# Optimization experiments

Measured on AMD Instinct MI355X. Metric: run time of the kernel, lower is better.

The kernel has to match this reference:

```python
import jax, jax.numpy as jnp
import numpy as np

DIM = 1024
H = 16
DH = DIM // H
SCALE = DH ** -0.5
EPS = 1e-5


def _linear_params(key, fan_in, fan_out):
    k1, k2 = jax.random.split(key)
    bound = 1.0 / np.sqrt(fan_in)
    w = jax.random.uniform(k1, (fan_out, fan_in), jnp.float32, -bound, bound)
    b = jax.random.uniform(k2, (fan_out,), jnp.float32, -bound, bound)
    return w, b


def setup_inputs() -> dict:
    key = jax.random.key(0)
    ks = jax.random.split(key, 16)
    M, K, S_txt, S_img = 32, 128, 1024, 768
    inp = {
        'entity_text': jax.random.normal(ks[0], (M, K, DIM), jnp.float32),
        'entity_image': jax.random.normal(ks[1], (M, K, DIM), jnp.float32),
        'img_feat': jax.random.normal(ks[2], (M, S_img, DIM), jnp.float32),
        'txt_feat': jax.random.normal(ks[3], (M, S_txt, DIM), jnp.float32),
    }
    img_mask = jax.random.randint(ks[4], (M, S_img), 0, 2, jnp.int32)
    txt_mask = jax.random.randint(ks[5], (M, S_txt), 0, 2, jnp.int32)
    # guarantee at least one valid kv token per row (avoids all -inf rows)
    inp['img_mask'] = img_mask.at[:, 0].set(1)
    inp['txt_mask'] = txt_mask.at[:, 0].set(1)
    names = ['wq_t', 'wk_t', 'wv_t', 'wo_t', 'wq_i', 'wk_i', 'wv_i', 'wo_i']
    for i, n in enumerate(names):
        w, b = _linear_params(ks[6 + i], DIM, DIM)
        inp[n] = w
        inp['b' + n[1:]] = b
    inp['g_t'] = jnp.ones((DIM,), jnp.float32)
    inp['beta_t'] = jnp.zeros((DIM,), jnp.float32)
    inp['g_i'] = jnp.ones((DIM,), jnp.float32)
    inp['beta_i'] = jnp.zeros((DIM,), jnp.float32)
    return inp


def _attend(wq, bq, wk, bk, wv, bv, wo, bo, queries, kv, kv_mask):
    M, K, D = queries.shape
    S = kv.shape[1]
    Q = (queries @ wq.T + bq).reshape(M, K, H, DH)
    Kt = (kv @ wk.T + bk).reshape(M, S, H, DH)
    V = (kv @ wv.T + bv).reshape(M, S, H, DH)
    attn = jnp.einsum('mkhd,mshd->mhks', Q, Kt) * SCALE  # [M,H,K,S]
    attn = jnp.where(kv_mask[:, None, None, :] > 0, attn, -jnp.inf)
    attn = jax.nn.softmax(attn, axis=-1)
    attn = jnp.nan_to_num(attn, nan=0.0)  # dropout=eval mode (identity)
    out = jnp.einsum('mhks,mshd->mkhd', attn, V).reshape(M, K, D)
    return out @ wo.T + bo


def _layernorm(x, g, b):
    mu = jnp.mean(x, axis=-1, keepdims=True)
    var = jnp.mean(jnp.square(x - mu), axis=-1, keepdims=True)
    return (x - mu) * jax.lax.rsqrt(var + EPS) * g + b


def reference(entity_text, entity_image, img_feat, txt_feat, img_mask, txt_mask,
              wq_t, bq_t, wk_t, bk_t, wv_t, bv_t, wo_t, bo_t,
              wq_i, bq_i, wk_i, bk_i, wv_i, bv_i, wo_i, bo_i,
              g_t, beta_t, g_i, beta_i):
    out_t = _attend(wq_t, bq_t, wk_t, bk_t, wv_t, bv_t, wo_t, bo_t,
                    entity_text, txt_feat, txt_mask)
    out_i = _attend(wq_i, bq_i, wk_i, bk_i, wv_i, bv_i, wo_i, bo_i,
                    entity_image, img_feat, img_mask)
    et = _layernorm(entity_text + out_t, g_t, beta_t)
    ei = _layernorm(entity_image + out_i, g_i, beta_i)
    return (et, ei)
```

## Files before the change

kernel.cpp:

```cpp
#include <hip/hip_runtime.h>
#include <stdint.h>

typedef unsigned short u16;
typedef __attribute__((ext_vector_type(8))) short short8;
typedef __attribute__((ext_vector_type(4))) float f32x4;

#define SWZ(r) (((r) & 7) << 4)
#define SCALE 0.125f

__device__ __forceinline__ u16 f2bf(float f) {
  unsigned int x = __float_as_uint(f);
  x += 0x7fffu + ((x >> 16) & 1u);
  return (u16)(x >> 16);
}

__device__ __forceinline__ unsigned int cvtpk_bf16(float lo, float hi) {
  unsigned int r;
  asm("v_cvt_pk_bf16_f32 %0, %1, %2" : "=v"(r) : "v"(lo), "v"(hi));
  return r;
}

__device__ __forceinline__ f32x4 mfma16(short8 a, short8 b, f32x4 c) {
  return __builtin_amdgcn_mfma_f32_16x16x32_bf16(a, b, c, 0, 0, 0);
}

__device__ __forceinline__ void gload_lds16(const u16* g, u16* l) {
  __builtin_amdgcn_global_load_lds(
      (const __attribute__((address_space(1))) unsigned int*)g,
      (__attribute__((address_space(3))) unsigned int*)l, 16, 0, 0);
}

__device__ __forceinline__ int xcd_swz(int bid, int nwg) {
  int cpx = nwg >> 3;
  return (bid & 7) * cpx + (bid >> 3);
}

__device__ __forceinline__ void cvt8(const float* src, u16* dst) {
  float4 a = *(const float4*)src;
  float4 b = *(const float4*)(src + 4);
  uint4 u;
  u.x = cvtpk_bf16(a.x, a.y);
  u.y = cvtpk_bf16(a.z, a.w);
  u.z = cvtpk_bf16(b.x, b.y);
  u.w = cvtpk_bf16(b.z, b.w);
  *(uint4*)dst = u;
}

__global__ __launch_bounds__(256) void cvt_all_kernel(
    const float* __restrict__ w0, const float* __restrict__ w1,
    const float* __restrict__ w2, const float* __restrict__ w3,
    const float* __restrict__ ent, const float* __restrict__ feat,
    u16* __restrict__ Wbf, u16* __restrict__ entbf, u16* __restrict__ featbf,
    int nE8, int nF8) {
  const int nW8 = 524288;
  int total = nW8 + nE8 + nF8;
  int i = blockIdx.x * 256 + threadIdx.x;
  int stride = gridDim.x * 256;
  for (; i < total; i += stride) {
    if (i < nW8) {
      int mi = i >> 17;
      const float* s = (mi == 0) ? w0 : (mi == 1) ? w1 : (mi == 2) ? w2 : w3;
      size_t off = (size_t)(i & 131071) * 8;
      cvt8(s + off, Wbf + (size_t)mi * 1048576 + off);
    } else if (i < nW8 + nE8) {
      size_t off = (size_t)(i - nW8) * 8;
      cvt8(ent + off, entbf + off);
    } else {
      size_t off = (size_t)(i - nW8 - nE8) * 8;
      cvt8(feat + off, featbf + off);
    }
  }
}

__global__ __launch_bounds__(256) void cvt_a_kernel(
    const float* __restrict__ src, u16* __restrict__ dst, int n8) {
  int i = blockIdx.x * 256 + threadIdx.x;
  int stride = gridDim.x * 256;
  for (; i < n8; i += stride) cvt8(src + (size_t)i * 8, dst + (size_t)i * 8);
}

__device__ __forceinline__ void gemm_core_bf16(
    const u16* __restrict__ A, const u16* __restrict__ B,
    const float* __restrict__ bias0, const float* __restrict__ bias1,
    u16* __restrict__ C, int ldc, int bx, int by, u16* As, u16* Bs) {
  const int tid = threadIdx.x;
  const int lane = tid & 63;
  const int w = tid >> 6;
  const int wr = w >> 1, wc = w & 1;
  const int l15 = lane & 15, lg = lane >> 4;
  const int brow = by * 128;
  const int bcol = bx * 128;

  f32x4 acc[4][4] = {};

  for (int k0 = 0; k0 < 1024; k0 += 64) {
#pragma unroll
    for (int p = 0; p < 4; ++p) {
      int flat = p * 256 + tid;
      int row = flat >> 3;
      int cb = (flat & 7) * 16;
      int scb = cb ^ SWZ(row);
      gload_lds16(B + (size_t)(bcol + row) * 1024 + k0 + (scb >> 1),
                  Bs + (size_t)flat * 8);
    }
#pragma unroll
    for (int p = 0; p < 4; ++p) {
      int flat = p * 256 + tid;
      int row = flat >> 3;
      int cb = (flat & 7) * 16;
      int scb = cb ^ SWZ(row);
      gload_lds16(A + (size_t)(brow + row) * 1024 + k0 + (scb >> 1),
                  As + (size_t)flat * 8);
    }
    __syncthreads();

    short8 af[4][2], bfr[4][2];
#pragma unroll
    for (int i = 0; i < 4; ++i) {
#pragma unroll
      for (int kk = 0; kk < 2; ++kk) {
        int ar = wr * 64 + i * 16 + l15;
        af[i][kk] = *(const short8*)((const char*)As + ar * 128 +
                                     ((kk * 64 + lg * 16) ^ SWZ(ar)));
        int br = wc * 64 + i * 16 + l15;
        bfr[i][kk] = *(const short8*)((const char*)Bs + br * 128 +
                                      ((kk * 64 + lg * 16) ^ SWZ(br)));
      }
    }
#pragma unroll
    for (int i = 0; i < 4; ++i)
#pragma unroll
      for (int j = 0; j < 4; ++j)
#pragma unroll
        for (int kk = 0; kk < 2; ++kk)
          acc[i][j] = mfma16(af[i][kk], bfr[j][kk], acc[i][j]);
    __syncthreads();
  }

#pragma unroll
  for (int j = 0; j < 4; ++j) {
    int col = bcol + wc * 64 + j * 16 + l15;
    const float* bp = (col < 1024) ? bias0 : bias1;
    float bv = bp[col & 1023];
#pragma unroll
    for (int i = 0; i < 4; ++i) {
      int row0 = brow + wr * 64 + i * 16 + lg * 4;
#pragma unroll
      for (int r = 0; r < 4; ++r)
        C[(size_t)(row0 + r) * ldc + col] = f2bf(acc[i][j][r] + bv);
    }
  }
}

__global__ __launch_bounds__(256, 2) void qkv_gemm_kernel(
    const u16* __restrict__ A0, const u16* __restrict__ B0,
    const float* __restrict__ bq, u16* __restrict__ C0, int gx0, int nwg0,
    const u16* __restrict__ A1, const u16* __restrict__ B1,
    const float* __restrict__ bk, const float* __restrict__ bv,
    u16* __restrict__ C1, int gx1, int nwg1) {
  __shared__ __attribute__((aligned(16))) u16 As[128 * 64];
  __shared__ __attribute__((aligned(16))) u16 Bs[128 * 64];
  int bid = blockIdx.x;
  if (bid < nwg0) {
    int lid = xcd_swz(bid, nwg0);
    gemm_core_bf16(A0, B0, bq, bq, C0, 1024, lid % gx0, lid / gx0, As, Bs);
  } else {
    int lid = xcd_swz(bid - nwg0, nwg1);
    gemm_core_bf16(A1, B1, bk, bv, C1, 2048, lid % gx1, lid / gx1, As, Bs);
  }
}

template <bool A_F32, bool OUT_F32>
__global__ __launch_bounds__(256, 2) void gemm_bias_kernel(
    const void* __restrict__ Av, const u16* __restrict__ B,
    const float* __restrict__ bias0, const float* __restrict__ bias1,
    void* __restrict__ Cv, int ldc) {
  __shared__ __attribute__((aligned(16))) u16 As[128 * 64];
  __shared__ __attribute__((aligned(16))) u16 Bs[128 * 64];
  const int tid = threadIdx.x;
  const int lane = tid & 63;
  const int w = tid >> 6;
  const int wr = w >> 1, wc = w & 1;
  const int l15 = lane & 15, lg = lane >> 4;

  const int nwg = gridDim.x * gridDim.y;
  const int lid = xcd_swz(blockIdx.y * gridDim.x + blockIdx.x, nwg);
  const int bx = lid % gridDim.x;
  const int by = lid / gridDim.x;
  const int brow = by * 128;
  const int bcol = bx * 128;

  f32x4 acc[4][4] = {};

  for (int k0 = 0; k0 < 1024; k0 += 64) {
#pragma unroll
    for (int p = 0; p < 4; ++p) {
      int flat = p * 256 + tid;
      int row = flat >> 3;
      int cb = (flat & 7) * 16;
      int scb = cb ^ SWZ(row);
      gload_lds16(B + (size_t)(bcol + row) * 1024 + k0 + (scb >> 1),
                  Bs + (size_t)flat * 8);
    }
    if constexpr (A_F32) {
      const float* Af = (const float*)Av;
#pragma unroll
      for (int p = 0; p < 4; ++p) {
        int flat = p * 256 + tid;
        int row = flat >> 3;
        int c8 = flat & 7;
        const float* src = Af + (size_t)(brow + row) * 1024 + k0 + c8 * 8;
        float4 v0 = ((const float4*)src)[0];
        float4 v1 = ((const float4*)src)[1];
        uint4 u;
        u.x = cvtpk_bf16(v0.x, v0.y);
        u.y = cvtpk_bf16(v0.z, v0.w);
        u.z = cvtpk_bf16(v1.x, v1.y);
        u.w = cvtpk_bf16(v1.z, v1.w);
        *(uint4*)((char*)As + row * 128 + ((c8 * 16) ^ SWZ(row))) = u;
      }
    } else {
      const u16* Ab = (const u16*)Av;
#pragma unroll
      for (int p = 0; p < 4; ++p) {
        int flat = p * 256 + tid;
        int row = flat >> 3;
        int cb = (flat & 7) * 16;
        int scb = cb ^ SWZ(row);
        gload_lds16(Ab + (size_t)(brow + row) * 1024 + k0 + (scb >> 1),
                    As + (size_t)flat * 8);
      }
    }
    __syncthreads();

    short8 af[4][2], bfr[4][2];
#pragma unroll
    for (int i = 0; i < 4; ++i) {
#pragma unroll
      for (int kk = 0; kk < 2; ++kk) {
        int ar = wr * 64 + i * 16 + l15;
        af[i][kk] = *(const short8*)((const char*)As + ar * 128 +
                                     ((kk * 64 + lg * 16) ^ SWZ(ar)));
        int br = wc * 64 + i * 16 + l15;
        bfr[i][kk] = *(const short8*)((const char*)Bs + br * 128 +
                                      ((kk * 64 + lg * 16) ^ SWZ(br)));
      }
    }
#pragma unroll
    for (int i = 0; i < 4; ++i)
#pragma unroll
      for (int j = 0; j < 4; ++j)
#pragma unroll
        for (int kk = 0; kk < 2; ++kk)
          acc[i][j] = mfma16(af[i][kk], bfr[j][kk], acc[i][j]);
    __syncthreads();
  }

#pragma unroll
  for (int j = 0; j < 4; ++j) {
    int col = bcol + wc * 64 + j * 16 + l15;
    const float* bp = (col < 1024) ? bias0 : bias1;
    float bv = bp[col & 1023];
#pragma unroll
    for (int i = 0; i < 4; ++i) {
      int row0 = brow + wr * 64 + i * 16 + lg * 4;
#pragma unroll
      for (int r = 0; r < 4; ++r) {
        float v = acc[i][j][r] + bv;
        if constexpr (OUT_F32)
          ((float*)Cv)[(size_t)(row0 + r) * ldc + col] = v;
        else
          ((u16*)Cv)[(size_t)(row0 + r) * ldc + col] = f2bf(v);
      }
    }
  }
}

__global__ __launch_bounds__(256, 2) void attn_mfma_kernel(
    const u16* __restrict__ Q, const u16* __restrict__ KV,
    const int* __restrict__ mask, u16* __restrict__ AO, int S, int mbase) {
  __shared__ __attribute__((aligned(16))) u16 Ks[64 * 64];
  __shared__ __attribute__((aligned(16))) u16 Vt[64 * 64];
  __shared__ __attribute__((aligned(16))) u16 Ps[4 * 32 * 64];
  __shared__ float mb[64];

  const int tid = threadIdx.x;
  const int lane = tid & 63;
  const int w = tid >> 6;
  const int lid = xcd_swz(blockIdx.x, gridDim.x);
  const int ml = lid >> 4;
  const int h = lid & 15;
  const int mg = mbase + ml;
  const int l15 = lane & 15, lg = lane >> 4;

  short8 qf[2][2];
#pragma unroll
  for (int qb = 0; qb < 2; ++qb)
#pragma unroll
    for (int kk = 0; kk < 2; ++kk)
      qf[qb][kk] = *(const short8*)(Q + (size_t)(mg * 128 + w * 32 + qb * 16 + l15) * 1024 +
                                    h * 64 + kk * 32 + lg * 8);

  float mrun[2][4], lrun[2][4];
  f32x4 oacc[2][4] = {};
#pragma unroll
  for (int qb = 0; qb < 2; ++qb)
#pragma unroll
    for (int r = 0; r < 4; ++r) {
      mrun[qb][r] = -1e30f;
      lrun[qb][r] = 0.0f;
    }

  const size_t kvbase = (size_t)ml * S * 2048 + h * 64;

  for (int st = 0; st < S; st += 64) {
    if (tid < 64)
      mb[tid] = (mask[(size_t)mg * S + st + tid] > 0) ? 0.0f : -1e30f;
#pragma unroll
    for (int p = 0; p < 2; ++p) {
      int flat = p * 256 + tid;
      int row = flat >> 3;
      int c = flat & 7;
      short8 v = *(const short8*)(KV + kvbase + (size_t)(st + row) * 2048 + c * 8);
      *(short8*)((char*)Ks + row * 128 + ((c * 16) ^ SWZ(row))) = v;
    }
#pragma unroll
    for (int p = 0; p < 2; ++p) {
      int flat = p * 256 + tid;
      int srow = flat >> 3;
      int c = flat & 7;
      short8 v = *(const short8*)(KV + kvbase + 1024 + (size_t)(st + srow) * 2048 + c * 8);
#pragma unroll
      for (int j = 0; j < 8; ++j) {
        int dr = c * 8 + j;
        *(u16*)((char*)Vt + dr * 128 + ((srow * 2) ^ SWZ(dr))) = (u16)v[j];
      }
    }
    __syncthreads();

    short8 kf[4][2];
#pragma unroll
    for (int sb = 0; sb < 4; ++sb)
#pragma unroll
      for (int kk = 0; kk < 2; ++kk) {
        int row = sb * 16 + l15;
        kf[sb][kk] = *(const short8*)((const char*)Ks + row * 128 +
                                      ((kk * 64 + lg * 16) ^ SWZ(row)));
      }
    f32x4 sc[2][4] = {};
#pragma unroll
    for (int qb = 0; qb < 2; ++qb)
#pragma unroll
      for (int sb = 0; sb < 4; ++sb)
#pragma unroll
        for (int kk = 0; kk < 2; ++kk)
          sc[qb][sb] = mfma16(qf[qb][kk], kf[sb][kk], sc[qb][sb]);

    float mbv[4];
#pragma unroll
    for (int sb = 0; sb < 4; ++sb) mbv[sb] = mb[sb * 16 + l15];

#pragma unroll
    for (int qb = 0; qb < 2; ++qb) {
#pragma unroll
      for (int r = 0; r < 4; ++r) {
        float s0 = sc[qb][0][r] * SCALE + mbv[0];
        float s1 = sc[qb][1][r] * SCALE + mbv[1];
        float s2 = sc[qb][2][r] * SCALE + mbv[2];
        float s3 = sc[qb][3][r] * SCALE + mbv[3];
        float t = fmaxf(fmaxf(s0, s1), fmaxf(s2, s3));
        for (int d = 1; d < 16; d <<= 1) t = fmaxf(t, __shfl_xor(t, d));
        float mnew = fmaxf(mrun[qb][r], t);
        float resc = __expf(mrun[qb][r] - mnew);
        float p0 = __expf(s0 - mnew);
        float p1 = __expf(s1 - mnew);
        float p2 = __expf(s2 - mnew);
        float p3 = __expf(s3 - mnew);
        float rs = p0 + p1 + p2 + p3;
        for (int d = 1; d < 16; d <<= 1) rs += __shfl_xor(rs, d);
        lrun[qb][r] = lrun[qb][r] * resc + rs;
        mrun[qb][r] = mnew;
#pragma unroll
        for (int db = 0; db < 4; ++db) oacc[qb][db][r] *= resc;
        int row = qb * 16 + lg * 4 + r;
        char* pbase = (char*)Ps + (w * 32 + row) * 128;
        int colb = 2 * l15;
        *(u16*)(pbase + ((0 * 32 + colb) ^ SWZ(row))) = f2bf(p0);
        *(u16*)(pbase + ((1 * 32 + colb) ^ SWZ(row))) = f2bf(p1);
        *(u16*)(pbase + ((2 * 32 + colb) ^ SWZ(row))) = f2bf(p2);
        *(u16*)(pbase + ((3 * 32 + colb) ^ SWZ(row))) = f2bf(p3);
      }
    }
    __syncthreads();

    short8 pf[2][2], vf[4][2];
#pragma unroll
    for (int qb = 0; qb < 2; ++qb)
#pragma unroll
      for (int kk = 0; kk < 2; ++kk) {
        int row = qb * 16 + l15;
        pf[qb][kk] = *(const short8*)((const char*)Ps + (w * 32 + row) * 128 +
                                      ((kk * 64 + lg * 16) ^ SWZ(row)));
      }
#pragma unroll
    for (int db = 0; db < 4; ++db)
#pragma unroll
      for (int kk = 0; kk < 2; ++kk) {
        int row = db * 16 + l15;
        vf[db][kk] = *(const short8*)((const char*)Vt + row * 128 +
                                      ((kk * 64 + lg * 16) ^ SWZ(row)));
      }
#pragma unroll
    for (int qb = 0; qb < 2; ++qb)
#pragma unroll
      for (int db = 0; db < 4; ++db)
#pragma unroll
        for (int kk = 0; kk < 2; ++kk)
          oacc[qb][db] = mfma16(pf[qb][kk], vf[db][kk], oacc[qb][db]);
    __syncthreads();
  }

#pragma unroll
  for (int qb = 0; qb < 2; ++qb)
#pragma unroll
    for (int db = 0; db < 4; ++db)
#pragma unroll
      for (int r = 0; r < 4; ++r) {
        int grow = mg * 128 + w * 32 + qb * 16 + lg * 4 + r;
        int gcol = h * 64 + db * 16 + l15;
        float v = oacc[qb][db][r] / lrun[qb][r];
        AO[(size_t)grow * 1024 + gcol] = f2bf(v);
      }
}

__global__ __launch_bounds__(256) void ln_kernel(
    const float* __restrict__ X, const float* __restrict__ O,
    const float* __restrict__ g, const float* __restrict__ b,
    float* __restrict__ out) {
  int row = blockIdx.x;
  int tid = threadIdx.x;
  const float* xr = X + (size_t)row * 1024;
  const float* orr = O + (size_t)row * 1024;
  float4 xv = *(const float4*)(xr + tid * 4);
  float4 ov = *(const float4*)(orr + tid * 4);
  float v0 = xv.x + ov.x, v1 = xv.y + ov.y, v2 = xv.z + ov.z, v3 = xv.w + ov.w;
  float s = v0 + v1 + v2 + v3;
  float s2 = v0 * v0 + v1 * v1 + v2 * v2 + v3 * v3;
  for (int d = 1; d < 64; d <<= 1) {
    s += __shfl_xor(s, d);
    s2 += __shfl_xor(s2, d);
  }
  __shared__ float ps[4], ps2[4];
  int w = tid >> 6;
  if ((tid & 63) == 0) {
    ps[w] = s;
    ps2[w] = s2;
  }
  __syncthreads();
  s = ps[0] + ps[1] + ps[2] + ps[3];
  s2 = ps2[0] + ps2[1] + ps2[2] + ps2[3];
  float mu = s * (1.0f / 1024.0f);
  float var = s2 * (1.0f / 1024.0f) - mu * mu;
  float rstd = rsqrtf(var + 1e-5f);
  float4 gv = *(const float4*)(g + tid * 4);
  float4 bv = *(const float4*)(b + tid * 4);
  float4 ou;
  ou.x = (v0 - mu) * rstd * gv.x + bv.x;
  ou.y = (v1 - mu) * rstd * gv.y + bv.y;
  ou.z = (v2 - mu) * rstd * gv.z + bv.z;
  ou.w = (v3 - mu) * rstd * gv.w + bv.w;
  *(float4*)(out + (size_t)row * 1024 + tid * 4) = ou;
}

extern "C" void kernel_launch(void* const* d_in, const int* in_sizes, int n_in,
                              void* d_out, int out_size, void* d_ws, size_t ws_size,
                              hipStream_t stream) {
  const float* ent_t = (const float*)d_in[0];
  const float* ent_i = (const float*)d_in[1];
  const float* img_feat = (const float*)d_in[2];
  const float* txt_feat = (const float*)d_in[3];
  const int* img_mask = (const int*)d_in[4];
  const int* txt_mask = (const int*)d_in[5];
  const float* W[8];
  const float* Bv[8];
  for (int i = 0; i < 8; ++i) {
    W[i] = (const float*)d_in[6 + 2 * i];
    Bv[i] = (const float*)d_in[7 + 2 * i];
  }
  const float* g_t = (const float*)d_in[22];
  const float* beta_t = (const float*)d_in[23];
  const float* g_i = (const float*)d_in[24];
  const float* beta_i = (const float*)d_in[25];
  float* out = (float*)d_out;

  int nc = 0;
  size_t Xt = 0;
  for (int t = 1; t <= 4; t <<= 1) {
    size_t x = 134217728ull / t;
    if ((32ull << 20) + x + x / 2 <= ws_size) { nc = t; Xt = x; break; }
  }

  char* ws = (char*)d_ws;
  u16* Wbf = (u16*)ws;
  u16* Qbf = (u16*)(ws + (8ull << 20));
  u16* AObf = (u16*)(ws + (16ull << 20));

  if (nc > 0) {
    u16* entbf = (u16*)(ws + (24ull << 20));
    u16* KVc = (u16*)(ws + (32ull << 20));
    u16* featbf = (u16*)(ws + (32ull << 20) + Xt);
    float* Of32 = (float*)(ws + (32ull << 20));
    const int mpc = 32 / nc;

    for (int mod = 0; mod < 2; ++mod) {
      const float* ent = mod ? ent_i : ent_t;
      const float* feat = mod ? img_feat : txt_feat;
      const int* msk = mod ? img_mask : txt_mask;
      int S = mod ? 768 : 1024;
      int crows = mpc * S;

      const u16* wq = Wbf + 0ull * 1048576;
      const u16* wkv = Wbf + 1ull * 1048576;
      const u16* wo = Wbf + 3ull * 1048576;
      const float* bq = Bv[mod * 4 + 0];
      const float* bk = Bv[mod * 4 + 1];
      const float* bvv = Bv[mod * 4 + 2];
      const float* bo = Bv[mod * 4 + 3];

      cvt_all_kernel<<<2048, 256, 0, stream>>>(
          W[mod * 4 + 0], W[mod * 4 + 1], W[mod * 4 + 2], W[mod * 4 + 3],
          ent, feat, Wbf, entbf, featbf, 4096 * 128, crows * 128);

      for (int c = 0; c < nc; ++c) {
        if (c > 0) {
          const float* featc = feat + (size_t)c * mpc * S * 1024;
          cvt_a_kernel<<<2048, 256, 0, stream>>>(featc, featbf, crows * 128);
        }
        int nwg0 = (c == 0) ? 256 : 0;
        int nwg1 = 16 * (crows / 128);
        qkv_gemm_kernel<<<nwg0 + nwg1, 256, 0, stream>>>(
            entbf, wq, bq, Qbf, 8, nwg0,
            featbf, wkv, bk, bvv, KVc, 16, nwg1);
        attn_mfma_kernel<<<mpc * 16, 256, 0, stream>>>(Qbf, KVc, msk, AObf, S, c * mpc);
      }

      gemm_bias_kernel<false, true><<<dim3(8, 32), 256, 0, stream>>>(
          AObf, wo, bo, bo, Of32, 1024);
      ln_kernel<<<4096, 256, 0, stream>>>(ent, Of32,
                                          mod ? g_i : g_t, mod ? beta_i : beta_t,
                                          out + (size_t)mod * 4194304);
    }
  } else {
    int ncf = 4;
    if (ws_size >= (152ull << 20)) ncf = 1;
    else if (ws_size >= (88ull << 20)) ncf = 2;
    u16* KVc = (u16*)(ws + (24ull << 20));
    float* Of32 = (float*)(ws + (24ull << 20));
    const int mpc = 32 / ncf;

    for (int mod = 0; mod < 2; ++mod) {
      const float* ent = mod ? ent_i : ent_t;
      const float* feat = mod ? img_feat : txt_feat;
      const int* msk = mod ? img_mask : txt_mask;
      int S = mod ? 768 : 1024;

      cvt_all_kernel<<<2048, 256, 0, stream>>>(
          W[mod * 4 + 0], W[mod * 4 + 1], W[mod * 4 + 2], W[mod * 4 + 3],
          ent, ent, Wbf, Qbf , Qbf, 0, 0);

      const u16* wq = Wbf + 0ull * 1048576;
      const u16* wkv = Wbf + 1ull * 1048576;
      const u16* wo = Wbf + 3ull * 1048576;
      const float* bq = Bv[mod * 4 + 0];
      const float* bk = Bv[mod * 4 + 1];
      const float* bvv = Bv[mod * 4 + 2];
      const float* bo = Bv[mod * 4 + 3];

      gemm_bias_kernel<true, false><<<dim3(8, 32), 256, 0, stream>>>(
          ent, wq, bq, bq, Qbf, 1024);

      int crows = mpc * S;
      for (int c = 0; c < ncf; ++c) {
        const float* featc = feat + (size_t)c * mpc * S * 1024;
        gemm_bias_kernel<true, false><<<dim3(16, crows / 128), 256, 0, stream>>>(
            featc, wkv, bk, bvv, KVc, 2048);
        attn_mfma_kernel<<<mpc * 16, 256, 0, stream>>>(Qbf, KVc, msk, AObf, S, c * mpc);
      }

      gemm_bias_kernel<false, true><<<dim3(8, 32), 256, 0, stream>>>(
          AObf, wo, bo, bo, Of32, 1024);
      ln_kernel<<<4096, 256, 0, stream>>>(ent, Of32,
                                          mod ? g_i : g_t, mod ? beta_i : beta_t,
                                          out + (size_t)mod * 4194304);
    }
  }
}
```

Before: 525.0 us.

## Replace fused QKV GEMM with 256x256-tile double-buffered KV GEMM kernel

Replaces the 128x128 single-buffered fused Q+KV GEMM with a dedicated KV projection kernel. It uses 256x256 tiles, 512 threads, 128KB of LDS split into two buffers, and a staged prefetch schedule with explicit waitcnt, barriers and setprio around the MFMA quadrants. The Q projection moves to a separate gemm_bias_kernel launch. The aim is better operand reuse and overlap of global loads with MFMA work in the dominant KV GEMM. In exchange, Q no longer overlaps with KV, and occupancy is lower because of the large LDS footprint.

```diff
diff --git a/kernel.cpp b/kernel.cpp
--- a/kernel.cpp
+++ b/kernel.cpp
@@ -79,95 +79,148 @@
   for (; i < n8; i += stride) cvt8(src + (size_t)i * 8, dst + (size_t)i * 8);
 }
 
-__device__ __forceinline__ void gemm_core_bf16(
+__global__ __launch_bounds__(512, 2) void kv_gemm256_kernel(
     const u16* __restrict__ A, const u16* __restrict__ B,
     const float* __restrict__ bias0, const float* __restrict__ bias1,
-    u16* __restrict__ C, int ldc, int bx, int by, u16* As, u16* Bs) {
+    u16* __restrict__ C, int ldc, int gx) {
+  __shared__ __attribute__((aligned(16))) u16 lds[65536];
   const int tid = threadIdx.x;
   const int lane = tid & 63;
-  const int w = tid >> 6;
-  const int wr = w >> 1, wc = w & 1;
+  const int wid = tid >> 6;
+  const int wm = wid >> 2, wn = wid & 3;
   const int l15 = lane & 15, lg = lane >> 4;
-  const int brow = by * 128;
-  const int bcol = bx * 128;
-
-  f32x4 acc[4][4] = {};
-
-  for (int k0 = 0; k0 < 1024; k0 += 64) {
-#pragma unroll
-    for (int p = 0; p < 4; ++p) {
-      int flat = p * 256 + tid;
-      int row = flat >> 3;
-      int cb = (flat & 7) * 16;
-      int scb = cb ^ SWZ(row);
-      gload_lds16(B + (size_t)(bcol + row) * 1024 + k0 + (scb >> 1),
-                  Bs + (size_t)flat * 8);
-    }
-#pragma unroll
-    for (int p = 0; p < 4; ++p) {
-      int flat = p * 256 + tid;
-      int row = flat >> 3;
-      int cb = (flat & 7) * 16;
-      int scb = cb ^ SWZ(row);
-      gload_lds16(A + (size_t)(brow + row) * 1024 + k0 + (scb >> 1),
-                  As + (size_t)flat * 8);
-    }
-    __syncthreads();
-
-    short8 af[4][2], bfr[4][2];
-#pragma unroll
-    for (int i = 0; i < 4; ++i) {
-#pragma unroll
-      for (int kk = 0; kk < 2; ++kk) {
-        int ar = wr * 64 + i * 16 + l15;
-        af[i][kk] = *(const short8*)((const char*)As + ar * 128 +
-                                     ((kk * 64 + lg * 16) ^ SWZ(ar)));
-        int br = wc * 64 + i * 16 + l15;
-        bfr[i][kk] = *(const short8*)((const char*)Bs + br * 128 +
-                                      ((kk * 64 + lg * 16) ^ SWZ(br)));
-      }
-    }
-#pragma unroll
-    for (int i = 0; i < 4; ++i)
-#pragma unroll
-      for (int j = 0; j < 4; ++j)
-#pragma unroll
-        for (int kk = 0; kk < 2; ++kk)
-          acc[i][j] = mfma16(af[i][kk], bfr[j][kk], acc[i][j]);
-    __syncthreads();
+  const int lid = xcd_swz(blockIdx.x, gridDim.x);
+  const int bx = lid % gx, by = lid / gx;
+  const int brow = by * 256, bcol = bx * 256;
+
+  f32x4 acc[8][4] = {};
+  short8 af[4][2], bf[2][2][2];
+
+#define BARR __builtin_amdgcn_s_barrier()
+#define LGKM0 asm volatile("s_waitcnt lgkmcnt(0)" ::: "memory")
+#define VM4 asm volatile("s_waitcnt vmcnt(4)" ::: "memory")
+#define VM0 asm volatile("s_waitcnt vmcnt(0)" ::: "memory")
+
+#define STAGE_A(BUF, K0)                                                     \
+  {                                                                          \
+    u16* dst = lds + (BUF) * 32768;                                          \
+    _Pragma("unroll") for (int p = 0; p < 4; ++p) {                          \
+      int flat = p * 512 + tid;                                              \
+      int row = flat >> 3;                                                   \
+      int scb = ((flat & 7) * 16) ^ SWZ(row);                                \
+      gload_lds16(A + (size_t)(brow + row) * 1024 + (K0) + (scb >> 1),       \
+                  dst + (size_t)flat * 8);                                   \
+    }                                                                        \
+  }
+
+#define STAGE_B_HALF(BUF, K0, H)                                             \
+  {                                                                          \
+    u16* dst = lds + (BUF) * 32768 + 16384 + (H) * 8192;                     \
+    _Pragma("unroll") for (int p = 0; p < 2; ++p) {                          \
+      int flat = p * 512 + tid;                                              \
+      int row = (H) * 128 + (flat >> 3);                                     \
+      int scb = ((flat & 7) * 16) ^ SWZ(row);                                \
+      gload_lds16(B + (size_t)(bcol + row) * 1024 + (K0) + (scb >> 1),       \
+                  dst + (size_t)flat * 8);                                   \
+    }                                                                        \
+  }
+
+#define READ_A(BUF, QM)                                                      \
+  {                                                                          \
+    const char* base_ = (const char*)(lds + (BUF) * 32768);                  \
+    _Pragma("unroll") for (int i = 0; i < 4; ++i)                            \
+        _Pragma("unroll") for (int kk = 0; kk < 2; ++kk) {                   \
+      int row = wm * 128 + (QM) * 64 + i * 16 + l15;                         \
+      af[i][kk] = *(const short8*)(base_ + row * 128 +                       \
+                                   ((kk * 64 + lg * 16) ^ SWZ(row)));        \
+    }                                                                        \
+  }
+
+#define READ_B(BUF, QN)                                                      \
+  {                                                                          \
+    const char* base_ = (const char*)(lds + (BUF) * 32768 + 16384);          \
+    _Pragma("unroll") for (int j = 0; j < 2; ++j)                            \
+        _Pragma("unroll") for (int kk = 0; kk < 2; ++kk) {                   \
+      int row = wn * 64 + (QN) * 32 + j * 16 + l15;                          \
+      bf[QN][j][kk] = *(const short8*)(base_ + row * 128 +                   \
+                                       ((kk * 64 + lg * 16) ^ SWZ(row)));    \
+    }                                                                        \
+  }
+
+#define MMAC(QM, QN)                                                         \
+  _Pragma("unroll") for (int i = 0; i < 4; ++i)                              \
+      _Pragma("unroll") for (int j = 0; j < 2; ++j)                          \
+          _Pragma("unroll") for (int kk = 0; kk < 2; ++kk)                   \
+              acc[(QM) * 4 + i][(QN) * 2 + j] =                              \
+      mfma16(af[i][kk], bf[QN][j][kk], acc[(QM) * 4 + i][(QN) * 2 + j]);
+
+  STAGE_A(0, 0);
+  STAGE_B_HALF(0, 0, 0);
+  STAGE_B_HALF(0, 0, 1);
+  STAGE_A(1, 64);
+  VM4;
+  BARR;
+
+  for (int J = 0; J < 16; ++J) {
+    int buf = J & 1;
+    READ_A(buf, 0);
+    READ_B(buf, 0);
+    if (J < 15) STAGE_B_HALF(buf ^ 1, (J + 1) * 64, 0);
+    BARR;
+    LGKM0;
+    __builtin_amdgcn_s_setprio(1);
+    MMAC(0, 0);
+    __builtin_amdgcn_s_setprio(0);
+    BARR;
+    READ_B(buf, 1);
+    if (J < 15) STAGE_B_HALF(buf ^ 1, (J + 1) * 64, 1);
+    BARR;
+    LGKM0;
+    __builtin_amdgcn_s_setprio(1);
+    MMAC(0, 1);
+    __builtin_amdgcn_s_setprio(0);
+    BARR;
+    READ_A(buf, 1);
+    BARR;
+    LGKM0;
+    __builtin_amdgcn_s_setprio(1);
+    MMAC(1, 0);
+    __builtin_amdgcn_s_setprio(0);
+    BARR;
+    if (J < 14) STAGE_A(buf, (J + 2) * 64);
+    __builtin_amdgcn_s_setprio(1);
+    MMAC(1, 1);
+    __builtin_amdgcn_s_setprio(0);
+    if (J < 14) {
+      VM4;
+    } else {
+      VM0;
+    }
+    BARR;
   }
 
 #pragma unroll
   for (int j = 0; j < 4; ++j) {
-    int col = bcol + wc * 64 + j * 16 + l15;
+    int col = bcol + wn * 64 + j * 16 + l15;
     const float* bp = (col < 1024) ? bias0 : bias1;
     float bv = bp[col & 1023];
 #pragma unroll
-    for (int i = 0; i < 4; ++i) {
-      int row0 = brow + wr * 64 + i * 16 + lg * 4;
+    for (int i = 0; i < 8; ++i) {
+      int row0 = brow + wm * 128 + i * 16 + lg * 4;
 #pragma unroll
       for (int r = 0; r < 4; ++r)
         C[(size_t)(row0 + r) * ldc + col] = f2bf(acc[i][j][r] + bv);
     }
   }
-}
-
-__global__ __launch_bounds__(256, 2) void qkv_gemm_kernel(
-    const u16* __restrict__ A0, const u16* __restrict__ B0,
-    const float* __restrict__ bq, u16* __restrict__ C0, int gx0, int nwg0,
-    const u16* __restrict__ A1, const u16* __restrict__ B1,
-    const float* __restrict__ bk, const float* __restrict__ bv,
-    u16* __restrict__ C1, int gx1, int nwg1) {
-  __shared__ __attribute__((aligned(16))) u16 As[128 * 64];
-  __shared__ __attribute__((aligned(16))) u16 Bs[128 * 64];
-  int bid = blockIdx.x;
-  if (bid < nwg0) {
-    int lid = xcd_swz(bid, nwg0);
-    gemm_core_bf16(A0, B0, bq, bq, C0, 1024, lid % gx0, lid / gx0, As, Bs);
-  } else {
-    int lid = xcd_swz(bid - nwg0, nwg1);
-    gemm_core_bf16(A1, B1, bk, bv, C1, 2048, lid % gx1, lid / gx1, As, Bs);
-  }
+#undef BARR
+#undef LGKM0
+#undef VM4
+#undef VM0
+#undef STAGE_A
+#undef STAGE_B_HALF
+#undef READ_A
+#undef READ_B
+#undef MMAC
 }
 
 template <bool A_F32, bool OUT_F32>
@@ -531,16 +584,17 @@
           W[mod * 4 + 0], W[mod * 4 + 1], W[mod * 4 + 2], W[mod * 4 + 3],
           ent, feat, Wbf, entbf, featbf, 4096 * 128, crows * 128);
 
+      gemm_bias_kernel<false, false><<<dim3(8, 32), 256, 0, stream>>>(
+          entbf, wq, bq, bq, Qbf, 1024);
+
       for (int c = 0; c < nc; ++c) {
         if (c > 0) {
           const float* featc = feat + (size_t)c * mpc * S * 1024;
           cvt_a_kernel<<<2048, 256, 0, stream>>>(featc, featbf, crows * 128);
         }
-        int nwg0 = (c == 0) ? 256 : 0;
-        int nwg1 = 16 * (crows / 128);
-        qkv_gemm_kernel<<<nwg0 + nwg1, 256, 0, stream>>>(
-            entbf, wq, bq, Qbf, 8, nwg0,
-            featbf, wkv, bk, bvv, KVc, 16, nwg1);
+        int nwg = (crows / 256) * 8;
+        kv_gemm256_kernel<<<nwg, 512, 0, stream>>>(
+            featbf, wkv, bk, bvv, KVc, 2048, 8);
         attn_mfma_kernel<<<mpc * 16, 256, 0, stream>>>(Qbf, KVc, msk, AObf, S, c * mpc);
       }
 
@@ -566,7 +620,7 @@
 
       cvt_all_kernel<<<2048, 256, 0, stream>>>(
           W[mod * 4 + 0], W[mod * 4 + 1], W[mod * 4 + 2], W[mod * 4 + 3],
-          ent, ent, Wbf, Qbf , Qbf, 0, 0);
+          ent, ent, Wbf, Qbf, Qbf, 0, 0);
 
       const u16* wq = Wbf + 0ull * 1048576;
       const u16* wkv = Wbf + 1ull * 1048576;
```

Measured after the change: 551.8 us. 1.05x slower.
